# Performance work log

Measured on AMD Instinct MI355X. Metric: run time of the kernel, lower is better.

Reference implementation:

```python
import jax, jax.numpy as jnp
import numpy as np

NN_SIZE = 10
EPS = 1e-8


def _knn_idx(x, k):
    # x: (B,N,3) -> idx: (B,N,k) indices of k nearest neighbors (incl. self)
    sq = jnp.sum(x * x, axis=-1)                     # (B,N)
    d = sq[:, :, None] + sq[:, None, :] - 2.0 * jnp.einsum('bnd,bmd->bnm', x, x)
    _, idx = jax.lax.top_k(-d, k)                    # (B,N,k)
    return idx


def _normals_from_idx(x, idx):
    # gather neighborhoods: (B,N,k,3)
    nbrs = jax.vmap(lambda pts, i: pts[i])(x, idx)
    centered = nbrs - jnp.mean(nbrs, axis=2, keepdims=True)
    # per-point 3x3 covariance
    cov = jnp.einsum('bnki,bnkj->bnij', centered, centered) / centered.shape[2]
    # eigenvector of smallest eigenvalue = PCA normal (eigh sorts ascending)
    _, vecs = jnp.linalg.eigh(cov)
    return vecs[..., :, 0]                           # (B,N,3)


def batch_normals(x, nn_size):
    idx = _knn_idx(x, nn_size)
    return _normals_from_idx(x, idx), idx


def setup_inputs() -> dict:
    key = jax.random.key(0)
    k1, k2, k3 = jax.random.split(key, 3)
    B, N = 4, 8192
    gt = jax.random.normal(k1, (B, N, 3), dtype=jnp.float32)
    pred = jax.random.normal(k2, (B, N, 3), dtype=jnp.float32)
    idx12 = jax.random.randint(k3, (B, N), 0, N, dtype=jnp.int64)
    return {"gt": gt, "pred": pred, "idx12": idx12}


def reference(gt, pred, idx12):
    gt_normals, _ = batch_normals(gt, NN_SIZE)
    # reorder pred by correspondence idx12, then estimate its normals
    pred_g = jnp.take_along_axis(pred, idx12[..., None].astype(jnp.int32).repeat(3, axis=-1), axis=1)
    pred_normals, _ = batch_normals(pred_g, NN_SIZE)
    # torch CosineSimilarity(dim=-1, eps=1e-8)
    dot = jnp.sum(pred_normals * gt_normals, axis=-1)
    denom = jnp.maximum(jnp.linalg.norm(pred_normals, axis=-1) * jnp.linalg.norm(gt_normals, axis=-1), EPS)
    loss = 1.0 - dot / denom
    return jnp.mean(loss)
```

## Files before the change

### kernel.cpp

```cpp
#include <hip/hip_runtime.h>
#include <math.h>

#define BB   4
#define NN   8192
#define BN   (BB*NN)
#define KNN  10
#define G    32
#define NCELLS (G*G*G)
#define GRID_LO (-5.0f)
#define H    0.3125f
#define INV_H 3.2f
#define RCAP 2

#define SEPS    5.9604645e-8f
#define SEPS2   (SEPS*SEPS)
#define SSAFMIN 1.1754944e-38f

__device__ __forceinline__ int cellc(float v) {
    int c = (int)floorf((v - GRID_LO) * INV_H);
    return min(G - 1, max(0, c));
}

__global__ __launch_bounds__(256) void prep_kernel(
    const float* __restrict__ gt, const float* __restrict__ pred,
    const unsigned* __restrict__ idxw, float4* __restrict__ P4,
    int* __restrict__ hist, float* __restrict__ accum,
    unsigned* __restrict__ counter, int* __restrict__ ovf_count)
{
    __shared__ int s_is32;
    int tid = threadIdx.x;
    if (tid == 0) s_is32 = 0;
    __syncthreads();
    if (idxw[2*tid + 1] != 0u) s_is32 = 1;
    __syncthreads();
    bool is64 = (s_is32 == 0);

    if (blockIdx.x == 0 && tid == 0) {
        *accum = 0.0f; *counter = 0u; *ovf_count = 0;
    }

    int point = blockIdx.x * 256 + tid;
    int pair = point >> 13;
    int r    = point & (NN - 1);
    float x, y, z;
    if (point < BN) {
        const float* s = gt + (size_t)point*3;
        x = s[0]; y = s[1]; z = s[2];
    } else {
        int rr = point - BN;
        int b = rr >> 13;
        unsigned idx = is64 ? idxw[2*(size_t)rr] : idxw[rr];
        const float* s = pred + ((size_t)b*NN + idx)*3;
        x = s[0]; y = s[1]; z = s[2];
    }
    P4[point] = make_float4(x, y, z, __int_as_float(r));
    int cell = (cellc(z)*G + cellc(y))*G + cellc(x);
    atomicAdd(&hist[(size_t)pair*NCELLS + cell], 1);
}

__global__ __launch_bounds__(1024) void scan_kernel(
    const int* __restrict__ hist, int2* __restrict__ combo)
{
    int cloud = blockIdx.x;
    int tid = threadIdx.x;
    int lane = tid & 63, wid = tid >> 6;
    const int* h = hist + (size_t)cloud * NCELLS;
    int2* cb = combo + (size_t)cloud * NCELLS;

    int loc[32];
    int base = tid * 32;
    const int4* h4 = (const int4*)(h + base);
    int sum = 0;
    #pragma unroll
    for (int i = 0; i < 8; ++i) {
        int4 a = h4[i];
        loc[4*i+0] = a.x; loc[4*i+1] = a.y; loc[4*i+2] = a.z; loc[4*i+3] = a.w;
        sum += a.x + a.y + a.z + a.w;
    }
    int v = sum;
    #pragma unroll
    for (int off = 1; off < 64; off <<= 1) {
        int o = __shfl_up(v, off, 64);
        if (lane >= off) v += o;
    }
    __shared__ int ws[16], wsx[16];
    if (lane == 63) ws[wid] = v;
    __syncthreads();
    if (tid < 16) {
        int acc = 0;
        for (int i = 0; i < tid; ++i) acc += ws[i];
        wsx[tid] = acc;
    }
    __syncthreads();
    int run = (v - sum) + wsx[wid];

    int4* cb4 = (int4*)(cb + base);
    #pragma unroll
    for (int i = 0; i < 16; ++i) {
        int4 o;
        o.x = run; o.y = loc[2*i];     run += loc[2*i];
        o.z = run; o.w = loc[2*i+1];   run += loc[2*i+1];
        cb4[i] = o;
    }
}

__global__ __launch_bounds__(256) void scatter_kernel(
    const float4* __restrict__ P4, int* __restrict__ hist,
    const int2* __restrict__ combo, float4* __restrict__ S)
{
    int point = blockIdx.x * 256 + threadIdx.x;
    float4 p = P4[point];
    int pair = point >> 13;
    int cell = (cellc(p.z)*G + cellc(p.y))*G + cellc(p.x);
    int old = atomicSub(&hist[(size_t)pair*NCELLS + cell], 1);
    int pos = combo[(size_t)pair*NCELLS + cell].x + old - 1;
    S[(size_t)pair*NN + pos] = p;
}

__device__ __forceinline__ float f_sign(float a, float b) {
    return copysignf(a, b);
}
__device__ __forceinline__ float slapy2(float x, float y) {
#pragma clang fp contract(off)
    float xa = fabsf(x), ya = fabsf(y);
    float w = fmaxf(xa, ya), z = fminf(xa, ya);
    if (z == 0.0f) return w;
    float t = z / w;
    return w * __fsqrt_rn(1.0f + t*t);
}
__device__ __forceinline__ void slartg_(float f, float g, float* cs, float* sn, float* r) {
#pragma clang fp contract(off)
    if (g == 0.0f)      { *cs = 1.0f; *sn = 0.0f; *r = f; }
    else if (f == 0.0f) { *cs = 0.0f; *sn = f_sign(1.0f, g); *r = fabsf(g); }
    else {
        float f1 = fabsf(f);
        float d = __fsqrt_rn(f*f + g*g);
        float p = 1.0f / d;
        *cs = f1 * p;
        *sn = g * f_sign(p, f);
        *r  = f_sign(d, f);
    }
}
__device__ void slaev2_(float a, float b, float c,
                        float* rt1, float* rt2, float* cs1, float* sn1) {
#pragma clang fp contract(off)
    float sm = a + c, df = a - c;
    float adf = fabsf(df);
    float tb = b + b;
    float ab = fabsf(tb);
    float acmx, acmn;
    if (fabsf(a) > fabsf(c)) { acmx = a; acmn = c; } else { acmx = c; acmn = a; }
    float rt;
    if (adf > ab)      { float t = ab/adf; rt = adf*__fsqrt_rn(1.0f + t*t); }
    else if (adf < ab) { float t = adf/ab; rt = ab*__fsqrt_rn(1.0f + t*t); }
    else               { rt = ab*__fsqrt_rn(2.0f); }
    int sgn1;
    if (sm < 0.0f)      { *rt1 = 0.5f*(sm - rt); sgn1 = -1;
                          *rt2 = (acmx / *rt1)*acmn - (b / *rt1)*b; }
    else if (sm > 0.0f) { *rt1 = 0.5f*(sm + rt); sgn1 = 1;
                          *rt2 = (acmx / *rt1)*acmn - (b / *rt1)*b; }
    else                { *rt1 = 0.5f*rt; *rt2 = -0.5f*rt; sgn1 = 1; }
    float cs; int sgn2;
    if (df >= 0.0f) { cs = df + rt; sgn2 = 1; } else { cs = df - rt; sgn2 = -1; }
    float acs = fabsf(cs);
    float c1, s1;
    if (acs > ab) { float ct = -tb/cs; s1 = 1.0f/__fsqrt_rn(1.0f + ct*ct); c1 = ct*s1; }
    else {
        if (ab == 0.0f) { c1 = 1.0f; s1 = 0.0f; }
        else { float tn = -cs/tb; c1 = 1.0f/__fsqrt_rn(1.0f + tn*tn); s1 = tn*c1; }
    }
    if (sgn1 == sgn2) { float tn = c1; c1 = -s1; s1 = tn; }
    *cs1 = c1; *sn1 = s1;
}

__device__ void eigh3_smallest(float c00, float c01, float c02,
                               float c11, float c12, float c22, float nv[3])
{
#pragma clang fp contract(off)
    float d[4], e[3], z[4][4];
    float tau1, v2 = 0.0f;
    float e1, d2, d3, e2;
    float alpha = c01, x = c02;
    if (x == 0.0f) {
        tau1 = 0.0f; e1 = alpha;
        d2 = c11; d3 = c22; e2 = c12;
    } else {
        float beta = -f_sign(slapy2(alpha, fabsf(x)), alpha);
        tau1 = (beta - alpha) / beta;
        v2 = x / (alpha - beta);
        e1 = beta;
        float w1 = tau1*(c11 + c12*v2);
        float w2 = tau1*(c12 + c22*v2);
        float al = -0.5f*tau1*(w1 + w2*v2);
        w1 = w1 + al;
        w2 = w2 + al*v2;
        d2 = (c11 - w1) - w1;
        e2 = (c12 - v2*w1) - w2;
        d3 = (c22 - v2*w2) - w2*v2;
    }
    d[1] = c00; d[2] = d2; d[3] = d3;
    e[1] = e1;  e[2] = e2;
    z[1][1] = 1.0f; z[1][2] = 0.0f; z[1][3] = 0.0f;
    z[2][1] = 0.0f; z[3][1] = 0.0f;
    z[2][2] = 1.0f - tau1;
    float mtv = -tau1*v2;
    z[2][3] = mtv; z[3][2] = mtv;
    z[3][3] = 1.0f + mtv*v2;

    const int n = 3, nm1 = 2;
    int l1 = 1, jtot = 0;
    const int nmaxit = 90;
    float cw[3], sw[3];
    int guard = 0;
    while (guard++ < 64) {
        if (l1 > n) break;
        if (l1 > 1) e[l1-1] = 0.0f;
        int m = n;
        if (l1 <= nm1) {
            for (int mi = l1; mi <= nm1; ++mi) {
                float tst = fabsf(e[mi]);
                if (tst == 0.0f) { m = mi; break; }
                if (tst <= (__fsqrt_rn(fabsf(d[mi]))*__fsqrt_rn(fabsf(d[mi+1])))*SEPS) {
                    e[mi] = 0.0f; m = mi; break;
                }
            }
        }
        int l = l1;
        int lsv = l, lend = m, lendsv = lend;
        l1 = m + 1;
        if (lend == l) continue;
        if (fabsf(d[lend]) < fabsf(d[l])) { lend = lsv; l = lendsv; }

        if (lend > l) {
            while (true) {
                int m_ = lend;
                if (l != lend) {
                    for (int mi = l; mi <= lend-1; ++mi) {
                        float em = e[mi];
                        float tst = em*em;
                        if (tst <= (SEPS2*fabsf(d[mi]))*fabsf(d[mi+1]) + SSAFMIN) { m_ = mi; break; }
                    }
                }
                if (m_ < lend) e[m_] = 0.0f;
                float p = d[l];
                if (m_ == l) {
                    d[l] = p; l = l + 1;
                    if (l <= lend) continue; else break;
                }
                if (m_ == l + 1) {
                    float rt1, rt2, cc, ss;
                    slaev2_(d[l], e[l], d[l+1], &rt1, &rt2, &cc, &ss);
                    for (int i = 1; i <= 3; ++i) {
                        float tmp = z[i][l+1];
                        z[i][l+1] = cc*tmp - ss*z[i][l];
                        z[i][l]   = ss*tmp + cc*z[i][l];
                    }
                    d[l] = rt1; d[l+1] = rt2; e[l] = 0.0f;
                    l = l + 2;
                    if (l <= lend) continue; else break;
                }
                if (jtot == nmaxit) break;
                jtot++;
                float g = (d[l+1] - p) / (2.0f*e[l]);
                float r = slapy2(g, 1.0f);
                g = d[m_] - p + (e[l] / (g + f_sign(r, g)));
                float s = 1.0f, c = 1.0f;
                p = 0.0f;
                for (int i = m_-1; i >= l; --i) {
                    float f = s*e[i];
                    float b = c*e[i];
                    slartg_(g, f, &c, &s, &r);
                    if (i != m_-1) e[i+1] = r;
                    g = d[i+1] - p;
                    r = (d[i] - g)*s + (2.0f*c)*b;
                    p = s*r;
                    d[i+1] = g + p;
                    g = c*r - b;
                    cw[i] = c; sw[i] = -s;
                }
                for (int j = m_-1; j >= l; --j) {
                    float cc = cw[j], ss = sw[j];
                    for (int i = 1; i <= 3; ++i) {
                        float tmp = z[i][j+1];
                        z[i][j+1] = cc*tmp - ss*z[i][j];
                        z[i][j]   = ss*tmp + cc*z[i][j];
                    }
                }
                d[l] = d[l] - p;
                e[l] = g;
            }
        } else {
            while (true) {
                int m_ = lend;
                if (l != lend) {
                    for (int mi = l; mi >= lend+1; --mi) {
                        float em = e[mi-1];
                        float tst = em*em;
                        if (tst <= (SEPS2*fabsf(d[mi]))*fabsf(d[mi-1]) + SSAFMIN) { m_ = mi; break; }
                    }
                }
                if (m_ > lend) e[m_-1] = 0.0f;
                float p = d[l];
                if (m_ == l) {
                    d[l] = p; l = l - 1;
                    if (l >= lend) continue; else break;
                }
                if (m_ == l - 1) {
                    float rt1, rt2, cc, ss;
                    slaev2_(d[l-1], e[l-1], d[l], &rt1, &rt2, &cc, &ss);
                    for (int i = 1; i <= 3; ++i) {
                        float tmp = z[i][l];
                        z[i][l]   = cc*tmp - ss*z[i][l-1];
                        z[i][l-1] = ss*tmp + cc*z[i][l-1];
                    }
                    d[l-1] = rt1; d[l] = rt2; e[l-1] = 0.0f;
                    l = l - 2;
                    if (l >= lend) continue; else break;
                }
                if (jtot == nmaxit) break;
                jtot++;
                float g = (d[l-1] - p) / (2.0f*e[l-1]);
                float r = slapy2(g, 1.0f);
                g = d[m_] - p + (e[l-1] / (g + f_sign(r, g)));
                float s = 1.0f, c = 1.0f;
                p = 0.0f;
                for (int i = m_; i <= l-1; ++i) {
                    float f = s*e[i];
                    float b = c*e[i];
                    slartg_(g, f, &c, &s, &r);
                    if (i != m_) e[i-1] = r;
                    g = d[i] - p;
                    r = (d[i+1] - g)*s + (2.0f*c)*b;
                    p = s*r;
                    d[i] = g + p;
                    g = c*r - b;
                    cw[i] = c; sw[i] = s;
                }
                for (int j = m_; j <= l-1; ++j) {
                    float cc = cw[j], ss = sw[j];
                    for (int i = 1; i <= 3; ++i) {
                        float tmp = z[i][j+1];
                        z[i][j+1] = cc*tmp - ss*z[i][j];
                        z[i][j]   = ss*tmp + cc*z[i][j];
                    }
                }
                d[l] = d[l] - p;
                e[l-1] = g;
            }
        }
    }
    for (int ii = 2; ii <= 3; ++ii) {
        int i = ii - 1, k = i;
        float p = d[i];
        for (int j = ii; j <= 3; ++j) if (d[j] < p) { k = j; p = d[j]; }
        if (k != i) {
            d[k] = d[i]; d[i] = p;
            for (int r2 = 1; r2 <= 3; ++r2) {
                float t = z[r2][i]; z[r2][i] = z[r2][k]; z[r2][k] = t;
            }
        }
    }
    nv[0] = z[1][1]; nv[1] = z[2][1]; nv[2] = z[3][1];
}

__device__ void cov_compute(const float4* __restrict__ cl,
                            const unsigned long long keys[KNN], float c[6])
{
#pragma clang fp contract(off)
    float px[KNN], py[KNN], pz[KNN];
    float sx = 0.f, sy = 0.f, sz = 0.f;
    #pragma unroll
    for (int s = 0; s < KNN; ++s) {
        int ni = (int)(unsigned)(keys[s] & 0xFFFFFFFFull);
        float4 np = cl[ni];
        px[s] = np.x; py[s] = np.y; pz[s] = np.z;
        sx = sx + px[s]; sy = sy + py[s]; sz = sz + pz[s];
    }
    float mx = sx / 10.0f, my = sy / 10.0f, mz = sz / 10.0f;
    float c00=0.f,c01=0.f,c02=0.f,c11=0.f,c12=0.f,c22=0.f;
    #pragma unroll
    for (int s = 0; s < KNN; ++s) {
        float dx = px[s]-mx, dy = py[s]-my, dz = pz[s]-mz;
        c00 = c00 + dx*dx; c01 = c01 + dx*dy; c02 = c02 + dx*dz;
        c11 = c11 + dy*dy; c12 = c12 + dy*dz; c22 = c22 + dz*dz;
    }
    c[0] = c00/10.0f; c[1] = c01/10.0f; c[2] = c02/10.0f;
    c[3] = c11/10.0f; c[4] = c12/10.0f; c[5] = c22/10.0f;
}

#define PROC(p) do { \
    float ddx = qx - (p).x, ddy = qy - (p).y, ddz = qz - (p).z; \
    float dd = fmaf(ddz, ddz, fmaf(ddy, ddy, ddx*ddx)); \
    unsigned long long key = \
        ((unsigned long long)__float_as_uint(dd) << 32) | \
        (unsigned)__float_as_int((p).w); \
    if (key < kgate) { \
        unsigned long long ck = key; \
        _Pragma("unroll") \
        for (int s = 0; s < KNN; ++s) { \
            unsigned long long ok2 = keys[s]; \
            bool sw = ok2 > ck; \
            keys[s] = sw ? ck : ok2; \
            ck      = sw ? ok2 : ck; \
        } \
        k9 = keys[KNN-1]; \
        kgate = (k9 < qbK) ? k9 : qbK; \
    } \
} while (0)

#define SEGPROC(bgn, end) do { \
    int _j = (bgn) + sub, _je = (end); \
    for (; _j + 4 < _je; _j += 8) { \
        float4 _p0 = cs[_j]; float4 _p1 = cs[_j+4]; \
        PROC(_p0); PROC(_p1); \
    } \
    if (_j < _je) { float4 _p0 = cs[_j]; PROC(_p0); } \
} while (0)

#define QEXCH() do { \
    unsigned long long _o1 = __shfl_xor(k9, 1, 4); \
    unsigned long long _m1 = (_o1 < k9) ? _o1 : k9; \
    unsigned long long _o2 = __shfl_xor(_m1, 2, 4); \
    unsigned long long _qm = (_o2 < _m1) ? _o2 : _m1; \
    qbK = _qm | 0xFFFFFFFFull; \
    kgate = (k9 < qbK) ? k9 : qbK; \
} while (0)

#define QMERGE() do { \
    unsigned long long fin[KNN]; \
    _Pragma("unroll") \
    for (int r = 0; r < KNN; ++r) { \
        unsigned long long m = keys[0]; \
        unsigned long long _o1 = __shfl_xor(m, 1, 4); m = (_o1 < m) ? _o1 : m; \
        unsigned long long _o2 = __shfl_xor(m, 2, 4); m = (_o2 < m) ? _o2 : m; \
        fin[r] = m; \
        bool own = (keys[0] == m); \
        _Pragma("unroll") \
        for (int t = 0; t < KNN-1; ++t) keys[t] = own ? keys[t+1] : keys[t]; \
        keys[KNN-1] = own ? 0xFFFFFFFFFFFFFFFFull : keys[KNN-1]; \
    } \
    _Pragma("unroll") \
    for (int s = 0; s < KNN; ++s) keys[s] = fin[s]; \
    k9 = keys[KNN-1]; \
} while (0)

__global__ __launch_bounds__(256) void knn_main_kernel(
    const float4* __restrict__ P4, const float4* __restrict__ S,
    const int2* __restrict__ combo, float4* __restrict__ Cov,
    int* __restrict__ ovf, unsigned long long* __restrict__ ovf_key,
    int* __restrict__ ovf_count)
{
    int b = blockIdx.x;
    int bb = ((b & 31) << 5) | (b >> 5);
    int tidg = bb * 256 + threadIdx.x;
    int qid  = tidg >> 2;
    int sub  = tidg & 3;
    int pair = qid >> 13;
    int spos = qid & (NN - 1);
    const float4* __restrict__ cl = P4 + (size_t)pair * NN;
    const float4* __restrict__ cs = S  + (size_t)pair * NN;
    const int2*   __restrict__ cb = combo + (size_t)pair * NCELLS;

    float4 q = cs[spos];
    float qx = q.x, qy = q.y, qz = q.z;
    int qi = __float_as_int(q.w);
    int qcx = cellc(qx), qcy = cellc(qy), qcz = cellc(qz);

    unsigned long long keys[KNN];
    #pragma unroll
    for (int s = 0; s < KNN; ++s) keys[s] = 0xFFFFFFFFFFFFFFFFull;
    unsigned long long k9    = 0xFFFFFFFFFFFFFFFFull;
    unsigned long long qbK   = 0xFFFFFFFFFFFFFFFFull;
    unsigned long long kgate = 0xFFFFFFFFFFFFFFFFull;

    int x0 = max(qcx - 1, 0), x1 = min(qcx + 1, G - 1);
    {
        const int DZ9[9] = { 0,  0,  0, -1,  1, -1, -1,  1,  1};
        const int DY9[9] = { 0,  1, -1,  0,  0, -1,  1, -1,  1};
        int rb[9], re[9];
        #pragma unroll
        for (int r = 0; r < 9; ++r) {
            int zz = qcz + DZ9[r], yy = qcy + DY9[r];
            rb[r] = 0; re[r] = 0;
            if ((unsigned)zz < G && (unsigned)yy < G) {
                int cbase = (zz*G + yy)*G;
                int2 a  = cb[cbase + x0];
                int2 b2 = cb[cbase + x1];
                rb[r] = a.x; re[r] = b2.x + b2.y;
            }
        }
        #pragma unroll
        for (int r = 0; r < 9; ++r) {
            SEGPROC(rb[r], re[r]);
            if (r == 0 || r == 2 || r == 4 || r == 6) QEXCH();
        }
    }

    QMERGE();
    const unsigned long long k9M = k9;
    float worstM = __uint_as_float((unsigned)(k9M >> 32));

    bool skip = (H*H > worstM);

    qbK   = 0xFFFFFFFFFFFFFFFFull;
    kgate = k9;
    if (!skip) {
        int xs0 = max(qcx - 2, 0), xs1 = min(qcx + 2, G - 1);
        const int SZ16[16] = {-2,-2,-2,-2,-2,  2, 2, 2, 2, 2, -1,-1, 0, 0, 1, 1};
        const int SY16[16] = {-2,-1, 0, 1, 2, -2,-1, 0, 1, 2, -2, 2,-2, 2,-2, 2};
        #pragma unroll
        for (int r = 0; r < 16; ++r) {
            int zz = qcz + SZ16[r], yy = qcy + SY16[r];
            if ((unsigned)zz < G && (unsigned)yy < G) {
                float loy = fmaf((float)yy, H, GRID_LO);
                float loz = fmaf((float)zz, H, GRID_LO);
                float py = fmaxf(0.0f, fmaxf(loy - qy, qy - (loy + H)));
                float pz = fmaxf(0.0f, fmaxf(loz - qz, qz - (loz + H)));
                float pyz = fmaf(pz, pz, py*py);
                if (!(pyz > worstM)) {
                    int cbase = (zz*G + yy)*G;
                    int2 a  = cb[cbase + xs0];
                    int2 b2 = cb[cbase + xs1];
                    SEGPROC(a.x, b2.x + b2.y);
                }
            }
        }
        const int CZ18[18] = {-1,-1,-1,-1,-1,-1,  0, 0, 0, 0, 0, 0,  1, 1, 1, 1, 1, 1};
        const int CY18[18] = {-1,-1, 0, 0, 1, 1, -1,-1, 0, 0, 1, 1, -1,-1, 0, 0, 1, 1};
        const int CX18[18] = {-2, 2,-2, 2,-2, 2, -2, 2,-2, 2,-2, 2, -2, 2,-2, 2,-2, 2};
        #pragma unroll
        for (int r = 0; r < 18; ++r) {
            int zz = qcz + CZ18[r], yy = qcy + CY18[r], xx = qcx + CX18[r];
            if ((unsigned)zz < G && (unsigned)yy < G && (unsigned)xx < G) {
                float lox = fmaf((float)xx, H, GRID_LO);
                float loy = fmaf((float)yy, H, GRID_LO);
                float loz = fmaf((float)zz, H, GRID_LO);
                float px = fmaxf(0.0f, fmaxf(lox - qx, qx - (lox + H)));
                float py = fmaxf(0.0f, fmaxf(loy - qy, qy - (loy + H)));
                float pz = fmaxf(0.0f, fmaxf(loz - qz, qz - (loz + H)));
                float m2 = fmaf(pz, pz, fmaf(py, py, px*px));
                if (!(m2 > worstM)) {
                    int2 a = cb[(zz*G + yy)*G + xx];
                    SEGPROC(a.x, a.x + a.y);
                }
            }
        }
    }

    if (!skip) {
        int ch = (k9 != k9M) ? 1 : 0;
        ch |= __shfl_xor(ch, 1, 4);
        ch |= __shfl_xor(ch, 2, 4);
        if (ch) QMERGE();
    }
    float worst_m = __uint_as_float((unsigned)(k9 >> 32));

    float bf = (float)RCAP * H;
    bool resolved = (bf*bf > worst_m);
    if (resolved && sub == 0) {
        float c[6];
        cov_compute(cl, keys, c);
        size_t o = ((size_t)pair*NN + qi)*2;
        Cov[o]   = make_float4(c[0], c[1], c[2], c[3]);
        Cov[o+1] = make_float4(c[4], c[5], 0.0f, 0.0f);
    } else if (!resolved && sub == 0) {
        int pos = atomicAdd(ovf_count, 1);
        ovf[pos] = (pair << 13) | qi;
        ovf_key[pos] = k9;
    }
}

#define BRUTE_BLOCKS 2048
__global__ __launch_bounds__(256) void brute_kernel(
    const float4* __restrict__ P4, const int* __restrict__ ovf,
    const unsigned long long* __restrict__ ovf_key,
    const int* __restrict__ ovf_count, float4* __restrict__ Cov)
{
    int tid = threadIdx.x;
    int lane = tid & 63;
    int wid = tid >> 6;
    int count = *ovf_count;

    for (int oi = blockIdx.x * 4 + wid; oi < count; oi += BRUTE_BLOCKS * 4) {
        int rec = ovf[oi];
        unsigned long long bound = ovf_key[oi];
        float bound_d = __uint_as_float((unsigned)(bound >> 32));
        int pair = rec >> 13;
        int qi = rec & (NN - 1);
        const float4* __restrict__ cl = P4 + (size_t)pair * NN;
        float4 q = cl[qi];
        float qx = q.x, qy = q.y, qz = q.z;

        unsigned long long keys[KNN];
        #pragma unroll
        for (int s = 0; s < KNN; ++s) keys[s] = 0xFFFFFFFFFFFFFFFFull;
        unsigned long long k9 = keys[KNN-1];

#define BPROC(p, jj) do { \
        float ddx = qx - (p).x, ddy = qy - (p).y, ddz = qz - (p).z; \
        float dd = fmaf(ddz, ddz, fmaf(ddy, ddy, ddx*ddx)); \
        if (!(dd > bound_d)) { \
            unsigned long long key = \
                ((unsigned long long)__float_as_uint(dd) << 32) | (unsigned)(jj); \
            if (key < k9) { \
                unsigned long long ck = key; \
                _Pragma("unroll") \
                for (int s = 0; s < KNN; ++s) { \
                    unsigned long long ok2 = keys[s]; \
                    bool sw = ok2 > ck; \
                    keys[s] = sw ? ck : ok2; \
                    ck      = sw ? ok2 : ck; \
                } \
                k9 = keys[KNN-1]; \
            } \
        } \
    } while (0)
        #pragma unroll 1
        for (int i = 0; i < NN/64; i += 4) {
            float4 p0 = cl[(i+0)*64 + lane];
            float4 p1 = cl[(i+1)*64 + lane];
            float4 p2 = cl[(i+2)*64 + lane];
            float4 p3 = cl[(i+3)*64 + lane];
            BPROC(p0, (i+0)*64 + lane);
            BPROC(p1, (i+1)*64 + lane);
            BPROC(p2, (i+2)*64 + lane);
            BPROC(p3, (i+3)*64 + lane);
        }
#undef BPROC

        unsigned long long fin[KNN];
        #pragma unroll
        for (int r = 0; r < KNN; ++r) {
            unsigned long long m = keys[0];
            #pragma unroll
            for (int off = 1; off < 64; off <<= 1) {
                unsigned long long o = __shfl_xor(m, off);
                m = (o < m) ? o : m;
            }
            fin[r] = m;
            if (keys[0] == m) {
                #pragma unroll
                for (int t = 0; t < KNN-1; ++t) keys[t] = keys[t+1];
                keys[KNN-1] = 0xFFFFFFFFFFFFFFFFull;
            }
        }

        if (lane == 0) {
            float c[6];
            cov_compute(cl, fin, c);
            size_t o = ((size_t)pair*NN + qi)*2;
            Cov[o]   = make_float4(c[0], c[1], c[2], c[3]);
            Cov[o+1] = make_float4(c[4], c[5], 0.0f, 0.0f);
        }
    }
}

__global__ __launch_bounds__(256) void eigh_loss_kernel(
    const float4* __restrict__ Cov, float* __restrict__ accum,
    unsigned* __restrict__ counter, float* __restrict__ out)
{
    int tid = threadIdx.x;
    int t = blockIdx.x * 256 + tid;
    int k = t >> 1;
    int cld = t & 1;
    size_t ci = ((size_t)(cld ? BN + k : k)) * 2;
    float4 a0 = Cov[ci], a1 = Cov[ci + 1];
    float n[3];
    eigh3_smallest(a0.x, a0.y, a0.z, a0.w, a1.x, a1.y, n);

    float ox = __shfl_xor(n[0], 1);
    float oy = __shfl_xor(n[1], 1);
    float oz = __shfl_xor(n[2], 1);

    float v = 0.0f;
    if (cld == 0) {
        float gx=n[0], gy=n[1], gz=n[2];
        float hx=ox,  hy=oy,  hz=oz;
        float dot = fmaf(gx,hx,fmaf(gy,hy,gz*hz));
        float ng  = sqrtf(fmaf(gx,gx,fmaf(gy,gy,gz*gz)));
        float nh  = sqrtf(fmaf(hx,hx,fmaf(hy,hy,hz*hz)));
        float den = fmaxf(ng*nh, 1e-8f);
        v = 1.0f - dot/den;
    }

    __shared__ float red[256];
    red[tid] = v;
    __syncthreads();
    for (int s = 128; s > 0; s >>= 1) {
        if (tid < s) red[tid] += red[tid+s];
        __syncthreads();
    }
    if (tid == 0) {
        atomicAdd(accum, red[0]);
        __threadfence();
        unsigned old = atomicAdd(counter, 1u);
        if (old == (unsigned)(2*BN/256 - 1)) {
            float tot = atomicAdd(accum, 0.0f);
            out[0] = tot * (1.0f/(float)BN);
        }
    }
}

extern "C" void kernel_launch(void* const* d_in, const int* in_sizes, int n_in,
                              void* d_out, int out_size, void* d_ws, size_t ws_size,
                              hipStream_t stream)
{
    (void)in_sizes; (void)n_in; (void)out_size; (void)ws_size;
    const float*    gt   = (const float*)d_in[0];
    const float*    pred = (const float*)d_in[1];
    const unsigned* idxw = (const unsigned*)d_in[2];
    float* out = (float*)d_out;

    char* w = (char*)d_ws;
    float4* P4   = (float4*)w;                         w += (size_t)2*BN*16;
    float4* S    = (float4*)w;                         w += (size_t)2*BN*16;
    int*    hist = (int*)w;                            w += (size_t)8*NCELLS*4;
    int2*   combo = (int2*)w;                          w += (size_t)8*NCELLS*8;
    float4* Cov  = (float4*)w;                         w += (size_t)2*BN*32;
    float*  accum = (float*)w;                         w += 16;
    unsigned* counter = (unsigned*)(accum + 1);
    int*    ovf_count = (int*)(accum + 2);
    int*    ovf  = (int*)w;                            w += (size_t)2*BN*4;
    unsigned long long* ovf_key = (unsigned long long*)w;  w += (size_t)2*BN*8;

    hipMemsetAsync(hist, 0, (size_t)8*NCELLS*4, stream);
    hipLaunchKernelGGL(prep_kernel,    dim3(2*BN/256), dim3(256),  0, stream,
                       gt, pred, idxw, P4, hist, accum, counter, ovf_count);
    hipLaunchKernelGGL(scan_kernel,    dim3(8),        dim3(1024), 0, stream,
                       hist, combo);
    hipLaunchKernelGGL(scatter_kernel, dim3(2*BN/256), dim3(256),  0, stream,
                       P4, hist, combo, S);
    hipLaunchKernelGGL(knn_main_kernel, dim3(2*BN*4/256), dim3(256), 0, stream,
                       P4, S, combo, Cov, ovf, ovf_key, ovf_count);
    hipLaunchKernelGGL(brute_kernel,   dim3(BRUTE_BLOCKS), dim3(256), 0, stream,
                       P4, ovf, ovf_key, ovf_count, Cov);
    hipLaunchKernelGGL(eigh_loss_kernel, dim3(2*BN/256), dim3(256), 0, stream,
                       Cov, accum, counter, out);
}
```

Measured before the change: 267.9 us.

## Split brute-force overflow kNN query across whole block with shared-memory merge

Each overflow query is now handled by a full 256-thread block instead of a single wavefront, so each thread scans 32 candidates rather than 128. Every wavefront does its own top-10 reduction, then thread 0 merges the four sorted lists from shared memory and computes the covariance. This shortens the per-query scan latency when there are few overflow queries, but adds two block barriers per query and cuts the number of queries processed at once by four.

Result: faster. 242.0 us (median of 2 runs) (-9.7%).

```diff
diff --git a/kernel.cpp b/kernel.cpp
--- a/kernel.cpp
+++ b/kernel.cpp
@@ -576,12 +576,13 @@
     const unsigned long long* __restrict__ ovf_key,
     const int* __restrict__ ovf_count, float4* __restrict__ Cov)
 {
+    __shared__ unsigned long long wl[4][KNN];
     int tid = threadIdx.x;
     int lane = tid & 63;
     int wid = tid >> 6;
     int count = *ovf_count;
 
-    for (int oi = blockIdx.x * 4 + wid; oi < count; oi += BRUTE_BLOCKS * 4) {
+    for (int oi = blockIdx.x; oi < count; oi += BRUTE_BLOCKS) {
         int rec = ovf[oi];
         unsigned long long bound = ovf_key[oi];
         float bound_d = __uint_as_float((unsigned)(bound >> 32));
@@ -616,15 +617,15 @@
         } \
     } while (0)
         #pragma unroll 1
-        for (int i = 0; i < NN/64; i += 4) {
-            float4 p0 = cl[(i+0)*64 + lane];
-            float4 p1 = cl[(i+1)*64 + lane];
-            float4 p2 = cl[(i+2)*64 + lane];
-            float4 p3 = cl[(i+3)*64 + lane];
-            BPROC(p0, (i+0)*64 + lane);
-            BPROC(p1, (i+1)*64 + lane);
-            BPROC(p2, (i+2)*64 + lane);
-            BPROC(p3, (i+3)*64 + lane);
+        for (int i = 0; i < 32; i += 4) {
+            float4 p0 = cl[(i+0)*256 + tid];
+            float4 p1 = cl[(i+1)*256 + tid];
+            float4 p2 = cl[(i+2)*256 + tid];
+            float4 p3 = cl[(i+3)*256 + tid];
+            BPROC(p0, (i+0)*256 + tid);
+            BPROC(p1, (i+1)*256 + tid);
+            BPROC(p2, (i+2)*256 + tid);
+            BPROC(p3, (i+3)*256 + tid);
         }
 #undef BPROC
 
@@ -646,12 +647,31 @@
         }
 
         if (lane == 0) {
+            #pragma unroll
+            for (int s = 0; s < KNN; ++s) wl[wid][s] = fin[s];
+        }
+        __syncthreads();
+        if (tid == 0) {
+            int i0 = 0, i1 = 0, i2 = 0, i3 = 0;
+            unsigned long long outk[KNN];
+            #pragma unroll
+            for (int r = 0; r < KNN; ++r) {
+                unsigned long long h0 = wl[0][i0], h1 = wl[1][i1];
+                unsigned long long h2 = wl[2][i2], h3 = wl[3][i3];
+                unsigned long long m01 = (h0 < h1) ? h0 : h1;
+                unsigned long long m23 = (h2 < h3) ? h2 : h3;
+                unsigned long long m   = (m01 < m23) ? m01 : m23;
+                outk[r] = m;
+                i0 += (h0 == m); i1 += (h1 == m);
+                i2 += (h2 == m); i3 += (h3 == m);
+            }
             float c[6];
-            cov_compute(cl, fin, c);
+            cov_compute(cl, outk, c);
             size_t o = ((size_t)pair*NN + qi)*2;
             Cov[o]   = make_float4(c[0], c[1], c[2], c[3]);
             Cov[o+1] = make_float4(c[4], c[5], 0.0f, 0.0f);
         }
+        __syncthreads();
     }
 }
 
```
